# Kernel tuning notes

Hardware: AMD Instinct MI355X
Metric: run time of the kernel (lower is better)

The kernel has to match this reference:

```python
import jax, jax.numpy as jnp
import numpy as np

SIG = 1000  # signal length hard-coded in the torch module

def _fourier_weights(n, conj):
    k, m = np.mgrid[0:n, 0:n]
    theta = 2.0 * np.pi * k * m / n
    sin_sign = 1.0 if conj else -1.0
    return np.hstack([np.cos(theta), sin_sign * np.sin(theta)]).astype(np.float32)  # (n, 2n)

def setup_inputs() -> dict:
    key = jax.random.key(0)
    k_x, k_w3, k_b3 = jax.random.split(key, 3)
    x = jax.random.normal(k_x, (8192, SIG), dtype=jnp.float32)
    filters = jnp.asarray(np.hamming(SIG), dtype=jnp.float32)[None, :]        # (1, 1000)
    Wf = jnp.asarray(_fourier_weights(SIG, conj=False))                        # (1000, 2000)
    Wfc = jnp.asarray(_fourier_weights(SIG, conj=True))                        # (1000, 2000)
    W3 = jax.random.normal(k_w3, (141, 500), dtype=jnp.float32)                # fc3 weight
    b3 = jax.random.normal(k_b3, (141,), dtype=jnp.float32) * 0.01             # fc3 bias
    return {"x": x, "filters": filters, "Wf": Wf, "Wfc": Wfc, "W3": W3, "b3": b3}

def reference(x, filters, Wf, Wfc, W3, b3):
    ham = x * filters                              # windowed signal, (B, 1000)
    out = ham @ Wf                                 # (B, 2000): [real | imag] of DFT
    out2 = ham @ Wfc                               # (B, 2000): [real | imag] of conj-DFT
    r1, i1 = out[:, :SIG], out[:, SIG:]
    r2, i2 = out2[:, :SIG], out2[:, SIG:]
    # |fft * fftconj| / 1000^2
    pr = r1 * r2 - i1 * i2
    pi = r1 * i2 + i1 * r2
    psd = jnp.sqrt(pr * pr + pi * pi) / (SIG ** 2)
    freq_probs = psd[:, :500] @ W3.T + b3          # (B, 141)
    return freq_probs
```

## Files before the change

### kernel.cpp

```cpp
#include <hip/hip_runtime.h>
#include <hip/hip_bf16.h>

#define SIG   1000
#define MROWS 8192
#define FK    512
#define FW    1024
#define NPAD  1024
#define PSDK  512
#define HN    192
#define NOUT  141
#define NT    16

using f32x4  = __attribute__((ext_vector_type(4))) float;
using short8 = __attribute__((ext_vector_type(8))) short;

__device__ inline ushort f2bf(float f) {
  union { float f; unsigned u; } v; v.f = f;
  unsigned u = v.u;
  unsigned r = (u + 0x7FFFu + ((u >> 16) & 1u)) >> 16;
  return (ushort)r;
}

__global__ __launch_bounds__(256) void prep_k(
    const float* __restrict__ x, const float* __restrict__ filt,
    const float* __restrict__ W3, ushort* __restrict__ fh,
    ushort* __restrict__ Bt, ushort* __restrict__ W3p) {
  const int tid = threadIdx.x;
  const int blk = blockIdx.x;
  if (blk < MROWS / 2) {
    const int r = blk * 2 + (tid >> 7);
    const int c = tid & 127;
    ushort4 e = make_ushort4(0, 0, 0, 0);
    ushort4 o = make_ushort4(0, 0, 0, 0);
    if (c < 125) {
      const float4* xr = (const float4*)(x + (size_t)r * SIG);
      const float4* fr = (const float4*)filt;
      const float4 xl = xr[c],       fl = fr[c];
      const float4 xh = xr[c + 125], fv = fr[c + 125];
      float lx = xl.x * fl.x, ly = xl.y * fl.y, lz = xl.z * fl.z, lw = xl.w * fl.w;
      float hx = xh.x * fv.x, hy = xh.y * fv.y, hz = xh.z * fv.z, hw = xh.w * fv.w;
      e.x = f2bf(lx + hx); e.y = f2bf(ly + hy); e.z = f2bf(lz + hz); e.w = f2bf(lw + hw);
      o.x = f2bf(lx - hx); o.y = f2bf(ly - hy); o.z = f2bf(lz - hz); o.w = f2bf(lw - hw);
    }
    ((ushort4*)(fh + (size_t)r * FW))[c]      = e;
    ((ushort4*)(fh + (size_t)r * FW + FK))[c] = o;
  } else {
    const int row = (blk - MROWS / 2) * 2 + (tid >> 7);
    const int c   = tid & 127;
    if (row < NPAD) {
      const int cg = row & 511, g = row >> 9;
      ushort4 o = make_ushort4(0, 0, 0, 0);
      if (cg < 500) {
        const int m = 2 * (cg >> 1) + g;
        const int trig = cg & 1;
        const float C = 6.28318530717958647692f / 1000.0f;
        ushort v[4];
#pragma unroll
        for (int j = 0; j < 4; ++j) {
          int ph = ((4 * c + j) * m) % 1000;
          float ang = ph * C;
          v[j] = f2bf(trig ? __sinf(ang) : __cosf(ang));
        }
        o = make_ushort4(v[0], v[1], v[2], v[3]);
      }
      ((ushort4*)(Bt + (size_t)row * FK))[c] = o;
    } else {
      const int n = row - NPAD;
      ushort4 o = make_ushort4(0, 0, 0, 0);
      if (n < NOUT && c < 125) {
        const float4 w = *(const float4*)(W3 + (size_t)n * 500 + 4 * c);
        o.x = f2bf(w.x); o.y = f2bf(w.y); o.z = f2bf(w.z); o.w = f2bf(w.w);
      }
      ((ushort4*)(W3p + (size_t)n * PSDK))[c] = o;
    }
  }
}

__global__ __launch_bounds__(256) void gemm_psd_k(
    const ushort* __restrict__ A, const ushort* __restrict__ Bt,
    ushort* __restrict__ psd) {
  __shared__ ushort lA[3][128 * 32];
  __shared__ ushort lB[3][128 * 32];
  const int tid  = threadIdx.x;
  const int wave = tid >> 6;
  const int lane = tid & 63;
  const int row0 = blockIdx.x * 128;
  const int n0   = blockIdx.y * 128;
  const int aoff = (blockIdx.y >= 4) ? FK : 0;
  const int wm = (wave >> 1) * 64;
  const int wn = (wave & 1) * 64;
  const int lr = lane & 15;
  const int kg = (lane >> 4) * 8;

  const int sb0   = wave * 2048;
  const int off0  = sb0 + lane * 16;
  const int row_0 = off0 >> 6;
  const int kb_0  = (off0 & 63) >> 1;
  const int off1  = off0 + 1024;
  const int row_1 = off1 >> 6;
  const int kb_1  = (off1 & 63) >> 1;
  const ushort* gA0 = A  + (size_t)(row0 + row_0) * FW + aoff + kb_0;
  const ushort* gA1 = A  + (size_t)(row0 + row_1) * FW + aoff + kb_1;
  const ushort* gB0 = Bt + (size_t)(n0 + row_0) * FK + kb_0;
  const ushort* gB1 = Bt + (size_t)(n0 + row_1) * FK + kb_1;

  f32x4 acc[4][4] = {};

#define STAGE(buf, k0)                                                          \
  do {                                                                          \
    __builtin_amdgcn_global_load_lds(                                           \
        (const __attribute__((address_space(1))) void*)(gA0 + (k0)),            \
        (__attribute__((address_space(3))) void*)((char*)lA[buf] + sb0), 16, 0, 0); \
    __builtin_amdgcn_global_load_lds(                                           \
        (const __attribute__((address_space(1))) void*)(gB0 + (k0)),            \
        (__attribute__((address_space(3))) void*)((char*)lB[buf] + sb0), 16, 0, 0); \
    __builtin_amdgcn_global_load_lds(                                           \
        (const __attribute__((address_space(1))) void*)(gA1 + (k0)),            \
        (__attribute__((address_space(3))) void*)((char*)lA[buf] + sb0 + 1024), 16, 0, 0); \
    __builtin_amdgcn_global_load_lds(                                           \
        (const __attribute__((address_space(1))) void*)(gB1 + (k0)),            \
        (__attribute__((address_space(3))) void*)((char*)lB[buf] + sb0 + 1024), 16, 0, 0); \
  } while (0)

  STAGE(0, 0);
  STAGE(1, 32);
  asm volatile("s_waitcnt vmcnt(4)" ::: "memory");
  __builtin_amdgcn_s_barrier();

#pragma unroll
  for (int kt = 0; kt < NT; ++kt) {
    const int cur = kt % 3;
    if (kt + 2 < NT) STAGE((kt + 2) % 3, (kt + 2) * 32);
    short8 a[4], b[4];
    const ushort* baseA = lA[cur];
    const ushort* baseB = lB[cur];
#pragma unroll
    for (int m = 0; m < 4; ++m)
      a[m] = *(const short8*)&baseA[(wm + m * 16 + lr) * 32 + kg];
#pragma unroll
    for (int n = 0; n < 4; ++n)
      b[n] = *(const short8*)&baseB[(wn + n * 16 + lr) * 32 + kg];
#pragma unroll
    for (int m = 0; m < 4; ++m)
#pragma unroll
      for (int n = 0; n < 4; ++n)
        acc[m][n] = __builtin_amdgcn_mfma_f32_16x16x32_bf16(a[m], b[n], acc[m][n], 0, 0, 0);
    if (kt < NT - 1) {
      if (kt + 2 < NT)
        asm volatile("s_waitcnt vmcnt(4) lgkmcnt(0)" ::: "memory");
      else
        asm volatile("s_waitcnt vmcnt(0) lgkmcnt(0)" ::: "memory");
      __builtin_amdgcn_s_barrier();
    }
  }
#undef STAGE

  const int g = blockIdx.y >> 2;
  const int colpar = lane & 1;
#pragma unroll
  for (int m = 0; m < 4; ++m) {
#pragma unroll
    for (int n = 0; n < 4; ++n) {
#pragma unroll
      for (int j = 0; j < 4; ++j) {
        float v  = acc[m][n][j];
        float v2 = __shfl_xor(v, 1);
        if (!colpar) {
          int grow  = row0 + wm + m * 16 + (lane >> 4) * 4 + j;
          int cg    = ((n0 + wn + n * 16 + lr) & 511);
          int mbin  = (cg & ~1) + g;
          psd[(size_t)grow * PSDK + mbin] = f2bf((v * v + v2 * v2) * 1e-6f);
        }
      }
    }
  }
}

__global__ __launch_bounds__(256) void head_gemm_k(
    const ushort* __restrict__ psd, const ushort* __restrict__ W3p,
    const float* __restrict__ b3, float* __restrict__ out) {
  __shared__ ushort lA[3][64 * 32];
  __shared__ ushort lB[3][HN * 32];
  const int tid  = threadIdx.x;
  const int wave = tid >> 6;
  const int lane = tid & 63;
  const int row0 = blockIdx.x * 64;
  const int wm = (wave >> 1) * 32;
  const int wn = (wave & 1) * 96;
  const int lr = lane & 15;
  const int kg = (lane >> 4) * 8;

  const int offA  = wave * 1024 + lane * 16;
  const int rowA  = offA >> 6;
  const int kbA   = (offA & 63) >> 1;
  const ushort* gA = psd + (size_t)(row0 + rowA) * PSDK + kbA;
  const int offB0 = wave * 3072 + lane * 16;
  const int rowB0 = offB0 >> 6,          kbB0 = (offB0 & 63) >> 1;
  const int rowB1 = (offB0 + 1024) >> 6, kbB1 = ((offB0 + 1024) & 63) >> 1;
  const int rowB2 = (offB0 + 2048) >> 6, kbB2 = ((offB0 + 2048) & 63) >> 1;
  const ushort* gB0 = W3p + (size_t)rowB0 * PSDK + kbB0;
  const ushort* gB1 = W3p + (size_t)rowB1 * PSDK + kbB1;
  const ushort* gB2 = W3p + (size_t)rowB2 * PSDK + kbB2;

  f32x4 acc[2][6] = {};

#define HSTAGE(buf, k0)                                                         \
  do {                                                                          \
    __builtin_amdgcn_global_load_lds(                                           \
        (const __attribute__((address_space(1))) void*)(gA + (k0)),             \
        (__attribute__((address_space(3))) void*)((char*)lA[buf] + wave * 1024), 16, 0, 0); \
    __builtin_amdgcn_global_load_lds(                                           \
        (const __attribute__((address_space(1))) void*)(gB0 + (k0)),            \
        (__attribute__((address_space(3))) void*)((char*)lB[buf] + wave * 3072), 16, 0, 0); \
    __builtin_amdgcn_global_load_lds(                                           \
        (const __attribute__((address_space(1))) void*)(gB1 + (k0)),            \
        (__attribute__((address_space(3))) void*)((char*)lB[buf] + wave * 3072 + 1024), 16, 0, 0); \
    __builtin_amdgcn_global_load_lds(                                           \
        (const __attribute__((address_space(1))) void*)(gB2 + (k0)),            \
        (__attribute__((address_space(3))) void*)((char*)lB[buf] + wave * 3072 + 2048), 16, 0, 0); \
  } while (0)

  HSTAGE(0, 0);
  HSTAGE(1, 32);
  asm volatile("s_waitcnt vmcnt(4)" ::: "memory");
  __builtin_amdgcn_s_barrier();

#pragma unroll
  for (int kt = 0; kt < NT; ++kt) {
    const int cur = kt % 3;
    if (kt + 2 < NT) HSTAGE((kt + 2) % 3, (kt + 2) * 32);
    short8 a[2], b[6];
    const ushort* baseA = lA[cur];
    const ushort* baseB = lB[cur];
#pragma unroll
    for (int m = 0; m < 2; ++m)
      a[m] = *(const short8*)&baseA[(wm + m * 16 + lr) * 32 + kg];
#pragma unroll
    for (int n = 0; n < 6; ++n)
      b[n] = *(const short8*)&baseB[(wn + n * 16 + lr) * 32 + kg];
#pragma unroll
    for (int m = 0; m < 2; ++m)
#pragma unroll
      for (int n = 0; n < 6; ++n)
        acc[m][n] = __builtin_amdgcn_mfma_f32_16x16x32_bf16(a[m], b[n], acc[m][n], 0, 0, 0);
    if (kt < NT - 1) {
      if (kt + 2 < NT)
        asm volatile("s_waitcnt vmcnt(4) lgkmcnt(0)" ::: "memory");
      else
        asm volatile("s_waitcnt vmcnt(0) lgkmcnt(0)" ::: "memory");
      __builtin_amdgcn_s_barrier();
    }
  }
#undef HSTAGE

#pragma unroll
  for (int m = 0; m < 2; ++m) {
#pragma unroll
    for (int n = 0; n < 6; ++n) {
#pragma unroll
      for (int j = 0; j < 4; ++j) {
        int gcol = wn + n * 16 + lr;
        if (gcol < NOUT) {
          int grow = row0 + wm + m * 16 + (lane >> 4) * 4 + j;
          out[(size_t)grow * NOUT + gcol] = acc[m][n][j] + b3[gcol];
        }
      }
    }
  }
}

extern "C" void kernel_launch(void* const* d_in, const int* in_sizes, int n_in,
                              void* d_out, int out_size, void* d_ws, size_t ws_size,
                              hipStream_t stream) {
  const float* x    = (const float*)d_in[0];
  const float* filt = (const float*)d_in[1];
  const float* W3   = (const float*)d_in[4];
  const float* b3   = (const float*)d_in[5];
  float* out = (float*)d_out;

  char* ws = (char*)d_ws;
  ushort* fh  = (ushort*)ws;
  ushort* Bt  = (ushort*)(ws + (size_t)MROWS * FW * 2);
  ushort* psd = (ushort*)(ws + (size_t)MROWS * FW * 2
                             + (size_t)NPAD * FK * 2);
  ushort* W3p = (ushort*)(ws + (size_t)MROWS * FW * 2
                             + (size_t)NPAD * FK * 2
                             + (size_t)MROWS * PSDK * 2);

  prep_k<<<MROWS / 2 + 608, 256, 0, stream>>>(x, filt, W3, fh, Bt, W3p);
  gemm_psd_k<<<dim3(MROWS / 128, NPAD / 128), 256, 0, stream>>>(fh, Bt, psd);
  head_gemm_k<<<MROWS / 64, 256, 0, stream>>>(psd, W3p, b3, out);
}
```

Baseline: 43.52 us.

## Shrink GEMM tiles, remap blocks per XCD, and add scheduling barriers

The PSD GEMM tile is halved to 64x128 and launched as a 1D grid whose block index is remapped so consecutive row tiles land on the same XCD. Load issue is spread as three LDS-direct loads per wave. The head GEMM now uses 16-row tiles with 512 blocks instead of 128, and waves split only the N dimension. Both kernels add sched_barrier fences around waitcnt and barrier points. The intent is more blocks to fill the CUs and better L2 locality, at the cost of more reloading of the B matrix and a lower MFMA-to-load ratio per tile.

```diff
diff --git a/kernel.cpp b/kernel.cpp
--- a/kernel.cpp
+++ b/kernel.cpp
@@ -20,6 +20,14 @@
   unsigned r = (u + 0x7FFFu + ((u >> 16) & 1u)) >> 16;
   return (ushort)r;
 }
+
+#define SYNC_BOUNDARY(WAITSTR)                         \
+  do {                                                 \
+    __builtin_amdgcn_sched_barrier(0);                 \
+    asm volatile(WAITSTR ::: "memory");                \
+    __builtin_amdgcn_s_barrier();                      \
+    __builtin_amdgcn_sched_barrier(0);                 \
+  } while (0)
 
 __global__ __launch_bounds__(256) void prep_k(
     const float* __restrict__ x, const float* __restrict__ filt,
@@ -76,89 +84,88 @@
   }
 }
 
-__global__ __launch_bounds__(256) void gemm_psd_k(
+__global__ __launch_bounds__(256, 4) void gemm_psd_k(
     const ushort* __restrict__ A, const ushort* __restrict__ Bt,
     ushort* __restrict__ psd) {
-  __shared__ ushort lA[3][128 * 32];
+  __shared__ ushort lA[3][64 * 32];
   __shared__ ushort lB[3][128 * 32];
   const int tid  = threadIdx.x;
   const int wave = tid >> 6;
   const int lane = tid & 63;
-  const int row0 = blockIdx.x * 128;
-  const int n0   = blockIdx.y * 128;
-  const int aoff = (blockIdx.y >= 4) ? FK : 0;
-  const int wm = (wave >> 1) * 64;
+  const int id  = blockIdx.x;
+  const int xcd = id & 7, rr = id >> 3;
+  const int bx  = xcd * 16 + (rr & 15);
+  const int by  = rr >> 4;
+  const int row0 = bx * 64;
+  const int n0   = by * 128;
+  const int aoff = (by >= 4) ? FK : 0;
+  const int wm = (wave >> 1) * 32;
   const int wn = (wave & 1) * 64;
   const int lr = lane & 15;
   const int kg = (lane >> 4) * 8;
 
-  const int sb0   = wave * 2048;
-  const int off0  = sb0 + lane * 16;
-  const int row_0 = off0 >> 6;
-  const int kb_0  = (off0 & 63) >> 1;
-  const int off1  = off0 + 1024;
-  const int row_1 = off1 >> 6;
-  const int kb_1  = (off1 & 63) >> 1;
-  const ushort* gA0 = A  + (size_t)(row0 + row_0) * FW + aoff + kb_0;
-  const ushort* gA1 = A  + (size_t)(row0 + row_1) * FW + aoff + kb_1;
-  const ushort* gB0 = Bt + (size_t)(n0 + row_0) * FK + kb_0;
-  const ushort* gB1 = Bt + (size_t)(n0 + row_1) * FK + kb_1;
-
-  f32x4 acc[4][4] = {};
-
-#define STAGE(buf, k0)                                                          \
-  do {                                                                          \
-    __builtin_amdgcn_global_load_lds(                                           \
-        (const __attribute__((address_space(1))) void*)(gA0 + (k0)),            \
-        (__attribute__((address_space(3))) void*)((char*)lA[buf] + sb0), 16, 0, 0); \
-    __builtin_amdgcn_global_load_lds(                                           \
-        (const __attribute__((address_space(1))) void*)(gB0 + (k0)),            \
-        (__attribute__((address_space(3))) void*)((char*)lB[buf] + sb0), 16, 0, 0); \
-    __builtin_amdgcn_global_load_lds(                                           \
-        (const __attribute__((address_space(1))) void*)(gA1 + (k0)),            \
-        (__attribute__((address_space(3))) void*)((char*)lA[buf] + sb0 + 1024), 16, 0, 0); \
-    __builtin_amdgcn_global_load_lds(                                           \
-        (const __attribute__((address_space(1))) void*)(gB1 + (k0)),            \
-        (__attribute__((address_space(3))) void*)((char*)lB[buf] + sb0 + 1024), 16, 0, 0); \
-  } while (0)
+  const ushort* gs[3];
+  int doff[3], isa[3];
+#pragma unroll
+  for (int j = 0; j < 3; ++j) {
+    const int i   = wave * 3 + j;
+    const int ia  = (i < 4);
+    const int idx = ia ? i : i - 4;
+    const int off = idx * 1024 + lane * 16;
+    const int row = off >> 6;
+    const int kb  = (off & 63) >> 1;
+    gs[j]   = ia ? (A  + (size_t)(row0 + row) * FW + aoff + kb)
+                 : (Bt + (size_t)(n0   + row) * FK + kb);
+    doff[j] = idx * 1024;
+    isa[j]  = ia;
+  }
+
+  auto STAGE = [&](int buf, int k0) {
+#pragma unroll
+    for (int j = 0; j < 3; ++j) {
+      char* db = (isa[j] ? (char*)lA[buf] : (char*)lB[buf]) + doff[j];
+      __builtin_amdgcn_global_load_lds(
+          (const __attribute__((address_space(1))) void*)(gs[j] + k0),
+          (__attribute__((address_space(3))) void*)db, 16, 0, 0);
+    }
+  };
+
+  f32x4 acc[2][4] = {};
 
   STAGE(0, 0);
   STAGE(1, 32);
-  asm volatile("s_waitcnt vmcnt(4)" ::: "memory");
-  __builtin_amdgcn_s_barrier();
+  SYNC_BOUNDARY("s_waitcnt vmcnt(3)");
 
 #pragma unroll
   for (int kt = 0; kt < NT; ++kt) {
     const int cur = kt % 3;
     if (kt + 2 < NT) STAGE((kt + 2) % 3, (kt + 2) * 32);
-    short8 a[4], b[4];
+    short8 a[2], b[4];
     const ushort* baseA = lA[cur];
     const ushort* baseB = lB[cur];
 #pragma unroll
-    for (int m = 0; m < 4; ++m)
+    for (int m = 0; m < 2; ++m)
       a[m] = *(const short8*)&baseA[(wm + m * 16 + lr) * 32 + kg];
 #pragma unroll
     for (int n = 0; n < 4; ++n)
       b[n] = *(const short8*)&baseB[(wn + n * 16 + lr) * 32 + kg];
 #pragma unroll
-    for (int m = 0; m < 4; ++m)
+    for (int m = 0; m < 2; ++m)
 #pragma unroll
       for (int n = 0; n < 4; ++n)
         acc[m][n] = __builtin_amdgcn_mfma_f32_16x16x32_bf16(a[m], b[n], acc[m][n], 0, 0, 0);
     if (kt < NT - 1) {
       if (kt + 2 < NT)
-        asm volatile("s_waitcnt vmcnt(4) lgkmcnt(0)" ::: "memory");
+        SYNC_BOUNDARY("s_waitcnt vmcnt(3) lgkmcnt(0)");
       else
-        asm volatile("s_waitcnt vmcnt(0) lgkmcnt(0)" ::: "memory");
-      __builtin_amdgcn_s_barrier();
-    }
-  }
-#undef STAGE
-
-  const int g = blockIdx.y >> 2;
+        SYNC_BOUNDARY("s_waitcnt vmcnt(0) lgkmcnt(0)");
+    }
+  }
+
+  const int g = by >> 2;
   const int colpar = lane & 1;
 #pragma unroll
-  for (int m = 0; m < 4; ++m) {
+  for (int m = 0; m < 2; ++m) {
 #pragma unroll
     for (int n = 0; n < 4; ++n) {
 #pragma unroll
@@ -166,9 +173,9 @@
         float v  = acc[m][n][j];
         float v2 = __shfl_xor(v, 1);
         if (!colpar) {
-          int grow  = row0 + wm + m * 16 + (lane >> 4) * 4 + j;
-          int cg    = ((n0 + wn + n * 16 + lr) & 511);
-          int mbin  = (cg & ~1) + g;
+          int grow = row0 + wm + m * 16 + (lane >> 4) * 4 + j;
+          int cg   = ((n0 + wn + n * 16 + lr) & 511);
+          int mbin = (cg & ~1) + g;
           psd[(size_t)grow * PSDK + mbin] = f2bf((v * v + v2 * v2) * 1e-6f);
         }
       }
@@ -176,94 +183,93 @@
   }
 }
 
-__global__ __launch_bounds__(256) void head_gemm_k(
+__global__ __launch_bounds__(256, 2) void head_gemm_k(
     const ushort* __restrict__ psd, const ushort* __restrict__ W3p,
     const float* __restrict__ b3, float* __restrict__ out) {
-  __shared__ ushort lA[3][64 * 32];
+  __shared__ ushort lA[3][16 * 32];
   __shared__ ushort lB[3][HN * 32];
   const int tid  = threadIdx.x;
   const int wave = tid >> 6;
   const int lane = tid & 63;
-  const int row0 = blockIdx.x * 64;
-  const int wm = (wave >> 1) * 32;
-  const int wn = (wave & 1) * 96;
+  const int row0 = blockIdx.x * 16;
+  const int wn = wave * 48;
   const int lr = lane & 15;
   const int kg = (lane >> 4) * 8;
 
-  const int offA  = wave * 1024 + lane * 16;
-  const int rowA  = offA >> 6;
-  const int kbA   = (offA & 63) >> 1;
-  const ushort* gA = psd + (size_t)(row0 + rowA) * PSDK + kbA;
-  const int offB0 = wave * 3072 + lane * 16;
-  const int rowB0 = offB0 >> 6,          kbB0 = (offB0 & 63) >> 1;
-  const int rowB1 = (offB0 + 1024) >> 6, kbB1 = ((offB0 + 1024) & 63) >> 1;
-  const int rowB2 = (offB0 + 2048) >> 6, kbB2 = ((offB0 + 2048) & 63) >> 1;
-  const ushort* gB0 = W3p + (size_t)rowB0 * PSDK + kbB0;
-  const ushort* gB1 = W3p + (size_t)rowB1 * PSDK + kbB1;
-  const ushort* gB2 = W3p + (size_t)rowB2 * PSDK + kbB2;
-
-  f32x4 acc[2][6] = {};
-
-#define HSTAGE(buf, k0)                                                         \
-  do {                                                                          \
-    __builtin_amdgcn_global_load_lds(                                           \
-        (const __attribute__((address_space(1))) void*)(gA + (k0)),             \
-        (__attribute__((address_space(3))) void*)((char*)lA[buf] + wave * 1024), 16, 0, 0); \
-    __builtin_amdgcn_global_load_lds(                                           \
-        (const __attribute__((address_space(1))) void*)(gB0 + (k0)),            \
-        (__attribute__((address_space(3))) void*)((char*)lB[buf] + wave * 3072), 16, 0, 0); \
-    __builtin_amdgcn_global_load_lds(                                           \
-        (const __attribute__((address_space(1))) void*)(gB1 + (k0)),            \
-        (__attribute__((address_space(3))) void*)((char*)lB[buf] + wave * 3072 + 1024), 16, 0, 0); \
-    __builtin_amdgcn_global_load_lds(                                           \
-        (const __attribute__((address_space(1))) void*)(gB2 + (k0)),            \
-        (__attribute__((address_space(3))) void*)((char*)lB[buf] + wave * 3072 + 2048), 16, 0, 0); \
-  } while (0)
+  const ushort* gs[4];
+  int doff[4], isa[4], valid[4];
+#pragma unroll
+  for (int j = 0; j < 4; ++j) {
+    const int i = wave + 4 * j;
+    valid[j] = (i < 13);
+    const int ia  = (i == 0);
+    const int idx = ia ? 0 : (i - 1);
+    const int off = (ia ? 0 : idx * 1024) + lane * 16;
+    const int row = off >> 6;
+    const int kb  = (off & 63) >> 1;
+    gs[j]   = ia ? (psd + (size_t)(row0 + row) * PSDK + kb)
+                 : (W3p + (size_t)row * PSDK + kb);
+    doff[j] = ia ? 0 : idx * 1024;
+    isa[j]  = ia;
+  }
+
+  auto HSTAGE = [&](int buf, int k0) {
+#pragma unroll
+    for (int j = 0; j < 4; ++j) {
+      if (valid[j]) {
+        char* db = (isa[j] ? (char*)lA[buf] : (char*)lB[buf]) + doff[j];
+        __builtin_amdgcn_global_load_lds(
+            (const __attribute__((address_space(1))) void*)(gs[j] + k0),
+            (__attribute__((address_space(3))) void*)db, 16, 0, 0);
+      }
+    }
+  };
+
+  f32x4 acc[3] = {};
 
   HSTAGE(0, 0);
   HSTAGE(1, 32);
-  asm volatile("s_waitcnt vmcnt(4)" ::: "memory");
+  __builtin_amdgcn_sched_barrier(0);
+  if (wave == 0) asm volatile("s_waitcnt vmcnt(4)" ::: "memory");
+  else           asm volatile("s_waitcnt vmcnt(3)" ::: "memory");
   __builtin_amdgcn_s_barrier();
+  __builtin_amdgcn_sched_barrier(0);
 
 #pragma unroll
   for (int kt = 0; kt < NT; ++kt) {
     const int cur = kt % 3;
     if (kt + 2 < NT) HSTAGE((kt + 2) % 3, (kt + 2) * 32);
-    short8 a[2], b[6];
+    short8 a, b[3];
     const ushort* baseA = lA[cur];
     const ushort* baseB = lB[cur];
-#pragma unroll
-    for (int m = 0; m < 2; ++m)
-      a[m] = *(const short8*)&baseA[(wm + m * 16 + lr) * 32 + kg];
-#pragma unroll
-    for (int n = 0; n < 6; ++n)
+    a = *(const short8*)&baseA[lr * 32 + kg];
+#pragma unroll
+    for (int n = 0; n < 3; ++n)
       b[n] = *(const short8*)&baseB[(wn + n * 16 + lr) * 32 + kg];
 #pragma unroll
-    for (int m = 0; m < 2; ++m)
-#pragma unroll
-      for (int n = 0; n < 6; ++n)
-        acc[m][n] = __builtin_amdgcn_mfma_f32_16x16x32_bf16(a[m], b[n], acc[m][n], 0, 0, 0);
+    for (int n = 0; n < 3; ++n)
+      acc[n] = __builtin_amdgcn_mfma_f32_16x16x32_bf16(a, b[n], acc[n], 0, 0, 0);
     if (kt < NT - 1) {
-      if (kt + 2 < NT)
-        asm volatile("s_waitcnt vmcnt(4) lgkmcnt(0)" ::: "memory");
-      else
+      __builtin_amdgcn_sched_barrier(0);
+      if (kt + 2 < NT) {
+        if (wave == 0) asm volatile("s_waitcnt vmcnt(4) lgkmcnt(0)" ::: "memory");
+        else           asm volatile("s_waitcnt vmcnt(3) lgkmcnt(0)" ::: "memory");
+      } else {
         asm volatile("s_waitcnt vmcnt(0) lgkmcnt(0)" ::: "memory");
+      }
       __builtin_amdgcn_s_barrier();
-    }
-  }
-#undef HSTAGE
-
-#pragma unroll
-  for (int m = 0; m < 2; ++m) {
-#pragma unroll
-    for (int n = 0; n < 6; ++n) {
-#pragma unroll
-      for (int j = 0; j < 4; ++j) {
-        int gcol = wn + n * 16 + lr;
-        if (gcol < NOUT) {
-          int grow = row0 + wm + m * 16 + (lane >> 4) * 4 + j;
-          out[(size_t)grow * NOUT + gcol] = acc[m][n][j] + b3[gcol];
-        }
+      __builtin_amdgcn_sched_barrier(0);
+    }
+  }
+
+#pragma unroll
+  for (int n = 0; n < 3; ++n) {
+#pragma unroll
+    for (int j = 0; j < 4; ++j) {
+      int gcol = wn + n * 16 + lr;
+      if (gcol < NOUT) {
+        int grow = row0 + (lane >> 4) * 4 + j;
+        out[(size_t)grow * NOUT + gcol] = acc[n][j] + b3[gcol];
       }
     }
   }
@@ -287,7 +293,7 @@
                              + (size_t)NPAD * FK * 2
                              + (size_t)MROWS * PSDK * 2);
 
-  prep_k<<<MROWS / 2 + 608, 256, 0, stream>>>(x, filt, W3, fh, Bt, W3p);
-  gemm_psd_k<<<dim3(MROWS / 128, NPAD / 128), 256, 0, stream>>>(fh, Bt, psd);
-  head_gemm_k<<<MROWS / 64, 256, 0, stream>>>(psd, W3p, b3, out);
-}
+  prep_k<<<MROWS / 2 + (NPAD + HN) / 2, 256, 0, stream>>>(x, filt, W3, fh, Bt, W3p);
+  gemm_psd_k<<<(MROWS / 64) * (NPAD / 128), 256, 0, stream>>>(fh, Bt, psd);
+  head_gemm_k<<<MROWS / 16, 256, 0, stream>>>(psd, W3p, b3, out);
+}
```

New measurement: 39.74 us. -8.7%, faster.
